# Optimization experiments

Measured on AMD Instinct MI355X. Metric: run time of the kernel, lower is better.

Reference implementation:

```python
import jax, jax.numpy as jnp
import numpy as np

H = 256
V = 10000
E = 300000


def setup_inputs() -> dict:
    key = jax.random.key(0)
    ks = jax.random.split(key, 7)
    s = 1.0 / np.sqrt(H)  # torch nn.Linear default init scale
    x = jax.random.normal(ks[0], (V, H), dtype=jnp.float32)
    e = jax.random.normal(ks[1], (E, H), dtype=jnp.float32)
    edge_index = jax.random.randint(ks[2], (2, E), 0, V, dtype=jnp.int64)
    Us_w = jax.random.uniform(ks[3], (H, H), dtype=jnp.float32, minval=-s, maxval=s)
    Us_b = jax.random.uniform(ks[4], (H,), dtype=jnp.float32, minval=-s, maxval=s)
    Vs_w = jax.random.uniform(ks[5], (H, H), dtype=jnp.float32, minval=-s, maxval=s)
    Vs_b = jax.random.uniform(ks[6], (H,), dtype=jnp.float32, minval=-s, maxval=s)
    return {"x": x, "e": e, "edge_index": edge_index,
            "Us_w": Us_w, "Us_b": Us_b, "Vs_w": Vs_w, "Vs_b": Vs_b}


def reference(x, e, edge_index, Us_w, Us_b, Vs_w, Vs_b):
    # Ue = Us(e): (E, H); Vx = Vs(x): (V, H)  [torch Linear: y = x @ W.T + b]
    Ue = jnp.einsum('eh,oh->eo', e, Us_w) + Us_b
    Vx = jnp.einsum('vh,oh->vo', x, Vs_w) + Vs_b
    src, dst = edge_index[0], edge_index[1]
    # gather + add epilogue: e_new = Ue + Vx[src] + Vx[dst]
    e_new = Ue + Vx[src] + Vx[dst]
    return e_new
```

## Files before the change

kernel.cpp:

```cpp
#include <hip/hip_runtime.h>


typedef __bf16 bf16_t;
typedef __bf16 bf16x4 __attribute__((ext_vector_type(4)));
typedef __bf16 bf16x8 __attribute__((ext_vector_type(8)));
typedef float f32x4 __attribute__((ext_vector_type(4)));
typedef float f32x8 __attribute__((ext_vector_type(8)));

#define HDIM 256
#define NV 10000
#define NE 300000

__device__ __forceinline__ void async16(const bf16_t* g, bf16_t* l) {
  __builtin_amdgcn_global_load_lds(
      (const __attribute__((address_space(1))) void*)g,
      (__attribute__((address_space(3))) void*)l, 16, 0, 0);
}

__global__ __launch_bounds__(256) void cvt_weights(
    const float* __restrict__ us, const float* __restrict__ vs,
    bf16_t* __restrict__ us_o, bf16_t* __restrict__ vs_o) {
  const int i = (blockIdx.x * 256 + threadIdx.x) * 4;
  f32x4 a = *(const f32x4*)(us + i);
  f32x4 b = *(const f32x4*)(vs + i);
  *(bf16x4*)(us_o + i) = __builtin_convertvector(a, bf16x4);
  *(bf16x4*)(vs_o + i) = __builtin_convertvector(b, bf16x4);
}

template <bool FUSED>
__global__ __launch_bounds__(256) void gemm(
    const float* __restrict__ A,
    const bf16_t* __restrict__ Wb,
    const float* __restrict__ bias,
    const int* __restrict__ sIdxG,
    const int* __restrict__ dIdxG,
    const bf16_t* __restrict__ Vx,
    float* __restrict__ outF,
    bf16_t* __restrict__ outB,
    int M) {
  __shared__ __align__(16) char smem[4 * 16 * 68 * 4];
  bf16_t* As = (bf16_t*)smem;
  bf16_t* Bs = (bf16_t*)(smem + 8192);
  __shared__ int sIdx[128];
  __shared__ int dIdx[128];

  const int tid = threadIdx.x;
  const int lane = tid & 63;
  const int wave = tid >> 6;
  const int wm = wave >> 1;
  const int wn = wave & 1;
  const int l15 = lane & 15;
  const int quad = lane >> 4;

  const int row0 = blockIdx.x * 128;
  const int n0 = blockIdx.y * 128;

  if (FUSED) {
    if (tid < 128) {
      int r = row0 + tid;
      if (r >= M) r = M - 1;
      sIdx[tid] = sIdxG[r];
    } else {
      int r = row0 + tid - 128;
      if (r >= M) r = M - 1;
      dIdx[tid - 128] = dIdxG[r];
    }
  }

  const int arow = tid >> 1;
  const int acol = (tid & 1) * 16;
  int garow = row0 + arow;
  if (garow >= M) garow = M - 1;
  const float* gA = A + (size_t)garow * HDIM + acol;
  bf16_t* lA = As + arow * 32 + acol;

  const bf16_t* gB0 = Wb + (size_t)(n0 + (tid >> 2)) * HDIM + (tid & 3) * 8;
  const bf16_t* gB1 = Wb + (size_t)(n0 + 64 + (tid >> 2)) * HDIM + (tid & 3) * 8;
  bf16_t* lB0 = Bs + tid * 8;
  bf16_t* lB1 = Bs + 2048 + tid * 8;

  f32x4 acc[4][4];
#pragma unroll
  for (int mi = 0; mi < 4; ++mi)
#pragma unroll
    for (int ni = 0; ni < 4; ++ni) {
      f32x4 z = {0.f, 0.f, 0.f, 0.f};
      acc[mi][ni] = z;
    }

  const int aBase = (wm * 64 + l15) * 32 + quad * 8;
  const int bBase = (wn * 64 + l15) * 32 + quad * 8;

  f32x4 pa0 = *(const f32x4*)(gA + 0);
  f32x4 pa1 = *(const f32x4*)(gA + 4);
  f32x4 pa2 = *(const f32x4*)(gA + 8);
  f32x4 pa3 = *(const f32x4*)(gA + 12);

  for (int k0 = 0; k0 < HDIM; k0 += 32) {
    async16(gB0 + k0, lB0);
    async16(gB1 + k0, lB1);

    f32x4 c0 = pa0, c1 = pa1, c2 = pa2, c3 = pa3;
    if (k0 + 32 < HDIM) {
      pa0 = *(const f32x4*)(gA + k0 + 32);
      pa1 = *(const f32x4*)(gA + k0 + 36);
      pa2 = *(const f32x4*)(gA + k0 + 40);
      pa3 = *(const f32x4*)(gA + k0 + 44);
    }
    f32x8 lo = {c0[0], c0[1], c0[2], c0[3], c1[0], c1[1], c1[2], c1[3]};
    f32x8 hi = {c2[0], c2[1], c2[2], c2[3], c3[0], c3[1], c3[2], c3[3]};
    *(bf16x8*)(lA + 0) = __builtin_convertvector(lo, bf16x8);
    *(bf16x8*)(lA + 8) = __builtin_convertvector(hi, bf16x8);

    __syncthreads();

    bf16x8 af[4], bfr[4];
#pragma unroll
    for (int mi = 0; mi < 4; ++mi)
      af[mi] = *(const bf16x8*)(As + aBase + mi * 16 * 32);
#pragma unroll
    for (int ni = 0; ni < 4; ++ni)
      bfr[ni] = *(const bf16x8*)(Bs + bBase + ni * 16 * 32);
#pragma unroll
    for (int mi = 0; mi < 4; ++mi)
#pragma unroll
      for (int ni = 0; ni < 4; ++ni)
        acc[mi][ni] = __builtin_amdgcn_mfma_f32_16x16x32_bf16(
            af[mi], bfr[ni], acc[mi][ni], 0, 0, 0);
    __syncthreads();
  }

  float bcol[4];
#pragma unroll
  for (int ni = 0; ni < 4; ++ni)
    bcol[ni] = bias[n0 + wn * 64 + ni * 16 + l15];

  float* stage = (float*)smem + wave * (16 * 68);
  const int srow = lane >> 2;
  const int scol = (lane & 3) * 4;

#pragma unroll
  for (int mi = 0; mi < 4; ++mi) {
#pragma unroll
    for (int ni = 0; ni < 4; ++ni)
#pragma unroll
      for (int r = 0; r < 4; ++r)
        stage[(quad * 4 + r) * 68 + ni * 16 + l15] = acc[mi][ni][r] + bcol[ni];

    const int rl = wm * 64 + mi * 16 + srow;
    const int row = row0 + rl;
    if (row < M) {
      const float* sp = stage + srow * 68;
      if (FUSED) {
        const bf16_t* vs = Vx + (size_t)sIdx[rl] * HDIM + n0 + wn * 64;
        const bf16_t* vd = Vx + (size_t)dIdx[rl] * HDIM + n0 + wn * 64;
        float* op = outF + (size_t)row * HDIM + n0 + wn * 64;
#pragma unroll
        for (int i = 0; i < 4; ++i) {
          const int c = i * 16 + scol;
          f32x4 a = *(const f32x4*)(sp + c);
          f32x4 sf = __builtin_convertvector(*(const bf16x4*)(vs + c), f32x4);
          f32x4 df = __builtin_convertvector(*(const bf16x4*)(vd + c), f32x4);
          *(f32x4*)(op + c) = a + sf + df;
        }
      } else {
        bf16_t* op = outB + (size_t)row * HDIM + n0 + wn * 64;
#pragma unroll
        for (int i = 0; i < 4; ++i) {
          const int c = i * 16 + scol;
          f32x4 a = *(const f32x4*)(sp + c);
          *(bf16x4*)(op + c) = __builtin_convertvector(a, bf16x4);
        }
      }
    }
  }
}

extern "C" void kernel_launch(void* const* d_in, const int* in_sizes, int n_in,
                              void* d_out, int out_size, void* d_ws,
                              size_t ws_size, hipStream_t stream) {
  const float* x = (const float*)d_in[0];
  const float* e = (const float*)d_in[1];
  const int* edge = (const int*)d_in[2];
  const float* Us_w = (const float*)d_in[3];
  const float* Us_b = (const float*)d_in[4];
  const float* Vs_w = (const float*)d_in[5];
  const float* Vs_b = (const float*)d_in[6];
  float* out = (float*)d_out;

  bf16_t* us_w_b = (bf16_t*)d_ws;
  bf16_t* vs_w_b = (bf16_t*)((char*)d_ws + (128 << 10));
  bf16_t* Vx = (bf16_t*)((char*)d_ws + (256 << 10));

  dim3 blk(256, 1, 1);

  cvt_weights<<<dim3(64, 1, 1), blk, 0, stream>>>(Us_w, Vs_w, us_w_b, vs_w_b);

  dim3 g1((NV + 127) / 128, 2, 1);
  gemm<false><<<g1, blk, 0, stream>>>(x, vs_w_b, Vs_b, nullptr, nullptr,
                                      nullptr, nullptr, Vx, NV);

  dim3 g2((NE + 127) / 128, 2, 1);
  gemm<true><<<g2, blk, 0, stream>>>(e, us_w_b, Us_b, edge, edge + NE, Vx, out,
                                     nullptr, NE);
}
```

Measured before the change: 611.1 us.

## Preload full weight half into LDS in MFMA fragment order, stream A via registers

The weight conversion kernel now writes bf16 weights pre-permuted into MFMA fragment order. Each GEMM block loads its entire 128xK weight half into 64KB of LDS once and reads A directly from global into registers, converting to bf16 in place. This removes the per-k-step A staging through LDS and the two barriers per iteration. The grid is reordered so the two column halves of the same rows run as adjacent blocks, which helps cache reuse of A and the gathered rows. The cost is 64KB of LDS per block, which limits occupancy, plus uncoalesced row-strided A loads from each lane.

```diff
diff --git a/kernel.cpp b/kernel.cpp
--- a/kernel.cpp
+++ b/kernel.cpp
@@ -20,11 +20,20 @@
 __global__ __launch_bounds__(256) void cvt_weights(
     const float* __restrict__ us, const float* __restrict__ vs,
     bf16_t* __restrict__ us_o, bf16_t* __restrict__ vs_o) {
-  const int i = (blockIdx.x * 256 + threadIdx.x) * 4;
-  f32x4 a = *(const f32x4*)(us + i);
-  f32x4 b = *(const f32x4*)(vs + i);
-  *(bf16x4*)(us_o + i) = __builtin_convertvector(a, bf16x4);
-  *(bf16x4*)(vs_o + i) = __builtin_convertvector(b, bf16x4);
+  const int c = blockIdx.x * 256 + threadIdx.x;
+  const int h = c >> 12;
+  const int g = (c >> 6) & 63;
+  const int ln = c & 63;
+  const int n = h * 128 + ((g >> 2) & 1) * 64 + (g & 3) * 16 + (ln & 15);
+  const int kb = (g >> 3) * 32 + (ln >> 4) * 8;
+  const float* su = us + n * HDIM + kb;
+  const float* sv = vs + n * HDIM + kb;
+  f32x4 a0 = *(const f32x4*)su, a1 = *(const f32x4*)(su + 4);
+  f32x4 b0 = *(const f32x4*)sv, b1 = *(const f32x4*)(sv + 4);
+  f32x8 av = {a0[0], a0[1], a0[2], a0[3], a1[0], a1[1], a1[2], a1[3]};
+  f32x8 bv = {b0[0], b0[1], b0[2], b0[3], b1[0], b1[1], b1[2], b1[3]};
+  *(bf16x8*)(us_o + c * 8) = __builtin_convertvector(av, bf16x8);
+  *(bf16x8*)(vs_o + c * 8) = __builtin_convertvector(bv, bf16x8);
 }
 
 template <bool FUSED>
@@ -38,11 +47,7 @@
     float* __restrict__ outF,
     bf16_t* __restrict__ outB,
     int M) {
-  __shared__ __align__(16) char smem[4 * 16 * 68 * 4];
-  bf16_t* As = (bf16_t*)smem;
-  bf16_t* Bs = (bf16_t*)(smem + 8192);
-  __shared__ int sIdx[128];
-  __shared__ int dIdx[128];
+  __shared__ __align__(16) char smem[65536];
 
   const int tid = threadIdx.x;
   const int lane = tid & 63;
@@ -52,32 +57,33 @@
   const int l15 = lane & 15;
   const int quad = lane >> 4;
 
-  const int row0 = blockIdx.x * 128;
-  const int n0 = blockIdx.y * 128;
-
-  if (FUSED) {
-    if (tid < 128) {
-      int r = row0 + tid;
-      if (r >= M) r = M - 1;
-      sIdx[tid] = sIdxG[r];
-    } else {
-      int r = row0 + tid - 128;
-      if (r >= M) r = M - 1;
-      dIdx[tid - 128] = dIdxG[r];
-    }
-  }
-
-  const int arow = tid >> 1;
-  const int acol = (tid & 1) * 16;
-  int garow = row0 + arow;
-  if (garow >= M) garow = M - 1;
-  const float* gA = A + (size_t)garow * HDIM + acol;
-  bf16_t* lA = As + arow * 32 + acol;
-
-  const bf16_t* gB0 = Wb + (size_t)(n0 + (tid >> 2)) * HDIM + (tid & 3) * 8;
-  const bf16_t* gB1 = Wb + (size_t)(n0 + 64 + (tid >> 2)) * HDIM + (tid & 3) * 8;
-  bf16_t* lB0 = Bs + tid * 8;
-  bf16_t* lB1 = Bs + 2048 + tid * 8;
+  const int n0 = blockIdx.x * 128;
+  const int row0 = blockIdx.y * 128;
+
+  const bf16_t* wsHalf = Wb + (size_t)blockIdx.x * 32768;
+  bf16_t* lB = (bf16_t*)smem;
+#pragma unroll
+  for (int i = 0; i < 16; ++i) {
+    const int c = tid + i * 256;
+    async16(wsHalf + c * 8, lB + c * 8);
+  }
+
+  const float* pA[4];
+#pragma unroll
+  for (int mi = 0; mi < 4; ++mi) {
+    int r = row0 + wm * 64 + mi * 16 + l15;
+    if (r >= M) r = M - 1;
+    pA[mi] = A + (size_t)r * HDIM + quad * 8;
+  }
+
+  f32x4 bufA[4][2], bufB[4][2];
+#pragma unroll
+  for (int mi = 0; mi < 4; ++mi) {
+    bufA[mi][0] = *(const f32x4*)(pA[mi] + 0);
+    bufA[mi][1] = *(const f32x4*)(pA[mi] + 4);
+    bufB[mi][0] = *(const f32x4*)(pA[mi] + 32);
+    bufB[mi][1] = *(const f32x4*)(pA[mi] + 36);
+  }
 
   f32x4 acc[4][4];
 #pragma unroll
@@ -88,47 +94,60 @@
       acc[mi][ni] = z;
     }
 
-  const int aBase = (wm * 64 + l15) * 32 + quad * 8;
-  const int bBase = (wn * 64 + l15) * 32 + quad * 8;
-
-  f32x4 pa0 = *(const f32x4*)(gA + 0);
-  f32x4 pa1 = *(const f32x4*)(gA + 4);
-  f32x4 pa2 = *(const f32x4*)(gA + 8);
-  f32x4 pa3 = *(const f32x4*)(gA + 12);
-
-  for (int k0 = 0; k0 < HDIM; k0 += 32) {
-    async16(gB0 + k0, lB0);
-    async16(gB1 + k0, lB1);
-
-    f32x4 c0 = pa0, c1 = pa1, c2 = pa2, c3 = pa3;
-    if (k0 + 32 < HDIM) {
-      pa0 = *(const f32x4*)(gA + k0 + 32);
-      pa1 = *(const f32x4*)(gA + k0 + 36);
-      pa2 = *(const f32x4*)(gA + k0 + 40);
-      pa3 = *(const f32x4*)(gA + k0 + 44);
-    }
-    f32x8 lo = {c0[0], c0[1], c0[2], c0[3], c1[0], c1[1], c1[2], c1[3]};
-    f32x8 hi = {c2[0], c2[1], c2[2], c2[3], c3[0], c3[1], c3[2], c3[3]};
-    *(bf16x8*)(lA + 0) = __builtin_convertvector(lo, bf16x8);
-    *(bf16x8*)(lA + 8) = __builtin_convertvector(hi, bf16x8);
-
-    __syncthreads();
-
-    bf16x8 af[4], bfr[4];
-#pragma unroll
-    for (int mi = 0; mi < 4; ++mi)
-      af[mi] = *(const bf16x8*)(As + aBase + mi * 16 * 32);
-#pragma unroll
-    for (int ni = 0; ni < 4; ++ni)
-      bfr[ni] = *(const bf16x8*)(Bs + bBase + ni * 16 * 32);
-#pragma unroll
-    for (int mi = 0; mi < 4; ++mi)
-#pragma unroll
-      for (int ni = 0; ni < 4; ++ni)
+  const int bOff = wn * 4096 + lane * 16;
+
+  __syncthreads();
+
+#pragma unroll 1
+  for (int i = 0; i < 4; ++i) {
+    const int k0 = i * 64;
+    bf16x8 af[4];
+#pragma unroll
+    for (int mi = 0; mi < 4; ++mi) {
+      f32x8 v = {bufA[mi][0][0], bufA[mi][0][1], bufA[mi][0][2], bufA[mi][0][3],
+                 bufA[mi][1][0], bufA[mi][1][1], bufA[mi][1][2], bufA[mi][1][3]};
+      af[mi] = __builtin_convertvector(v, bf16x8);
+    }
+    if (i < 3) {
+#pragma unroll
+      for (int mi = 0; mi < 4; ++mi) {
+        bufA[mi][0] = *(const f32x4*)(pA[mi] + k0 + 64);
+        bufA[mi][1] = *(const f32x4*)(pA[mi] + k0 + 68);
+      }
+    }
+#pragma unroll
+    for (int ni = 0; ni < 4; ++ni) {
+      bf16x8 bfr = *(const bf16x8*)(smem + (2 * i) * 8192 + ni * 1024 + bOff);
+#pragma unroll
+      for (int mi = 0; mi < 4; ++mi)
         acc[mi][ni] = __builtin_amdgcn_mfma_f32_16x16x32_bf16(
-            af[mi], bfr[ni], acc[mi][ni], 0, 0, 0);
-    __syncthreads();
-  }
+            af[mi], bfr, acc[mi][ni], 0, 0, 0);
+    }
+#pragma unroll
+    for (int mi = 0; mi < 4; ++mi) {
+      f32x8 v = {bufB[mi][0][0], bufB[mi][0][1], bufB[mi][0][2], bufB[mi][0][3],
+                 bufB[mi][1][0], bufB[mi][1][1], bufB[mi][1][2], bufB[mi][1][3]};
+      af[mi] = __builtin_convertvector(v, bf16x8);
+    }
+    if (i < 3) {
+#pragma unroll
+      for (int mi = 0; mi < 4; ++mi) {
+        bufB[mi][0] = *(const f32x4*)(pA[mi] + k0 + 96);
+        bufB[mi][1] = *(const f32x4*)(pA[mi] + k0 + 100);
+      }
+    }
+#pragma unroll
+    for (int ni = 0; ni < 4; ++ni) {
+      bf16x8 bfr =
+          *(const bf16x8*)(smem + (2 * i + 1) * 8192 + ni * 1024 + bOff);
+#pragma unroll
+      for (int mi = 0; mi < 4; ++mi)
+        acc[mi][ni] = __builtin_amdgcn_mfma_f32_16x16x32_bf16(
+            af[mi], bfr, acc[mi][ni], 0, 0, 0);
+    }
+  }
+
+  __syncthreads();
 
   float bcol[4];
 #pragma unroll
@@ -151,9 +170,11 @@
     const int row = row0 + rl;
     if (row < M) {
       const float* sp = stage + srow * 68;
-      if (FUSED) {
-        const bf16_t* vs = Vx + (size_t)sIdx[rl] * HDIM + n0 + wn * 64;
-        const bf16_t* vd = Vx + (size_t)dIdx[rl] * HDIM + n0 + wn * 64;
+      if constexpr (FUSED) {
+        const int si = sIdxG[row];
+        const int di = dIdxG[row];
+        const bf16_t* vs = Vx + (size_t)si * HDIM + n0 + wn * 64;
+        const bf16_t* vd = Vx + (size_t)di * HDIM + n0 + wn * 64;
         float* op = outF + (size_t)row * HDIM + n0 + wn * 64;
 #pragma unroll
         for (int i = 0; i < 4; ++i) {
@@ -194,13 +215,13 @@
 
   dim3 blk(256, 1, 1);
 
-  cvt_weights<<<dim3(64, 1, 1), blk, 0, stream>>>(Us_w, Vs_w, us_w_b, vs_w_b);
-
-  dim3 g1((NV + 127) / 128, 2, 1);
+  cvt_weights<<<dim3(32, 1, 1), blk, 0, stream>>>(Us_w, Vs_w, us_w_b, vs_w_b);
+
+  dim3 g1(2, (NV + 127) / 128, 1);
   gemm<false><<<g1, blk, 0, stream>>>(x, vs_w_b, Vs_b, nullptr, nullptr,
                                       nullptr, nullptr, Vx, NV);
 
-  dim3 g2((NE + 127) / 128, 2, 1);
+  dim3 g2(2, (NE + 127) / 128, 1);
   gemm<true><<<g2, blk, 0, stream>>>(e, us_w_b, Us_b, edge, edge + NE, Vx, out,
                                      nullptr, NE);
 }
```

After: 662.0 us. 1.08x slower.
